# Performance work log

Hardware: AMD Instinct MI355X
Metric: run time of the kernel (lower is better)

The kernel has to match this reference:

```python
import jax, jax.numpy as jnp
import numpy as np


def setup_inputs() -> dict:
    key = jax.random.key(0)
    ks = jax.random.split(key, 5)
    B, S, D = 2, 2048, 1024
    scale = 0.02
    return {
        "x": jax.random.normal(ks[0], (B, S, D), dtype=jnp.float32),
        "q_proj_weight": jax.random.normal(ks[1], (D, D), dtype=jnp.float32) * scale,
        "k_proj_weight": jax.random.normal(ks[2], (D, D), dtype=jnp.float32) * scale,
        "v_proj_weight": jax.random.normal(ks[3], (D, D), dtype=jnp.float32) * scale,
        "o_proj_weight": jax.random.normal(ks[4], (D, D), dtype=jnp.float32) * scale,
    }


def reference(x, q_proj_weight, k_proj_weight, v_proj_weight, o_proj_weight):
    num_heads = 16
    B, S, d_in = x.shape
    d_k = q_proj_weight.shape[0]
    head_size = d_k // num_heads

    def split_heads(t):  # [B,S,d_k] -> [B,H,S,hs]
        return t.reshape(B, S, num_heads, head_size).transpose(0, 2, 1, 3)

    q = split_heads(jnp.einsum('bsd,kd->bsk', x, q_proj_weight))
    k = split_heads(jnp.einsum('bsd,kd->bsk', x, k_proj_weight))
    v = split_heads(jnp.einsum('bsd,kd->bsk', x, v_proj_weight))

    scale = jnp.float32(head_size) ** -0.5
    scores = jnp.einsum('bhtc,bhkc->bhtk', q, k) * scale  # [B,H,S,S]
    causal = jnp.tril(jnp.ones((S, S), dtype=bool))
    scores = jnp.where(causal, scores, -jnp.inf)
    attn = jax.nn.softmax(scores, axis=-1)
    out = jnp.einsum('bhtk,bhkc->bhtc', attn, v)  # [B,H,S,hs]
    out = out.transpose(0, 2, 1, 3).reshape(B, S, d_k)
    return jnp.einsum('bsv,dv->bsd', out, o_proj_weight)
```

## Files before the change

### kernel.cpp

```cpp
#include <hip/hip_runtime.h>
#include <hip/hip_bf16.h>

typedef short bf16x8 __attribute__((ext_vector_type(8)));
typedef float f32x4 __attribute__((ext_vector_type(4)));

__device__ __forceinline__ short f2bf(float f) {
  union { __hip_bfloat16 h; short s; } u;
  u.h = __float2bfloat16(f);
  return u.s;
}

__device__ __forceinline__ void gload_lds16(const short* g, short* lds_base) {
  __builtin_amdgcn_global_load_lds(
      (const __attribute__((address_space(1))) void*)g,
      (__attribute__((address_space(3))) void*)lds_base, 16, 0, 0);
}

__global__ void cast_f32_bf16(const float* __restrict__ in, short* __restrict__ out, int n4) {
  int i = blockIdx.x * blockDim.x + threadIdx.x;
  if (i < n4) {
    float4 v = reinterpret_cast<const float4*>(in)[i];
    short4 o;
    o.x = f2bf(v.x); o.y = f2bf(v.y); o.z = f2bf(v.z); o.w = f2bf(v.w);
    reinterpret_cast<short4*>(out)[i] = o;
  }
}

__global__ void cast_w4(const float* __restrict__ w0, const float* __restrict__ w1,
                        const float* __restrict__ w2, const float* __restrict__ w3,
                        short* __restrict__ dst, int n4each) {
  int i = blockIdx.x * blockDim.x + threadIdx.x;
  if (i >= n4each) return;
  const float* src = (blockIdx.y == 0) ? w0 : (blockIdx.y == 1) ? w1
                   : (blockIdx.y == 2) ? w2 : w3;
  float4 v = reinterpret_cast<const float4*>(src)[i];
  short4 o;
  o.x = f2bf(v.x); o.y = f2bf(v.y); o.z = f2bf(v.z); o.w = f2bf(v.w);
  reinterpret_cast<short4*>(dst + (size_t)blockIdx.y * 1024 * 1024)[i] = o;
}

#define QSCALE 0.18033688f

template<int MODE>
__global__ __launch_bounds__(512, 1)
void gemm8p(const short* __restrict__ A, const short* __restrict__ Bw,
            short* __restrict__ Qo, short* __restrict__ Ko, short* __restrict__ Vo,
            float* __restrict__ Cf, int M, int N, int Kd)
{
  __shared__ short As[2][256 * 64];
  __shared__ short Bs[2][192 * 64];
  const int tid = threadIdx.x;
  const int wid = tid >> 6, lane = tid & 63;
  const int l16 = lane & 15, lq = lane >> 4;
  const int l = blockIdx.y * 16 + blockIdx.x;
  const int lsw = (l & 7) * 32 + (l >> 3);
  const int bm = (lsw & 15) * 256, bn = (lsw >> 4) * 192;
  const int wr = (wid >> 2) * 128;
  const int wc = (wid & 3) * 48;
  const int lrow = lane >> 3;
  const int scol = ((lane & 7) ^ lrow) * 8;

#define ST_A(slot, k0) do { _Pragma("unroll")                                     \
  for (int j = 0; j < 4; ++j) {                                                   \
    int r = j * 64 + wid * 8;                                                     \
    gload_lds16(A + (size_t)(bm + r + lrow) * Kd + (k0) + scol, &As[slot][r * 64]); } } while (0)
#define ST_B(slot, k0) do { _Pragma("unroll")                                     \
  for (int j = 0; j < 3; ++j) {                                                   \
    int r = j * 64 + wid * 8;                                                     \
    gload_lds16(Bw + (size_t)(bn + r + lrow) * Kd + (k0) + scol, &Bs[slot][r * 64]); } } while (0)

  f32x4 acc[8][3];
#pragma unroll
  for (int m = 0; m < 8; ++m)
#pragma unroll
    for (int n = 0; n < 3; ++n) acc[m][n] = (f32x4){0.f, 0.f, 0.f, 0.f};

  const int nt = Kd >> 6;
  ST_A(0, 0);  ST_B(0, 0);
  ST_A(1, 64); ST_B(1, 64);
  asm volatile("s_waitcnt vmcnt(7)" ::: "memory");
  __builtin_amdgcn_s_barrier();
  asm volatile("" ::: "memory");

  bf16x8 af[4][2], bl[2][2], bh1[2];

  for (int t = 0; t < nt; ++t) {
    const int slot = t & 1;
    const int k2 = (t + 2) << 6;
    const bool st = (t + 2) < nt;

#pragma unroll
    for (int ks = 0; ks < 2; ++ks) {
      const int csw = (ks * 32 + lq * 8) ^ ((l16 & 7) << 3);
#pragma unroll
      for (int m = 0; m < 4; ++m)
        af[m][ks] = *(const bf16x8*)&As[slot][(wr + m * 16 + l16) * 64 + csw];
#pragma unroll
      for (int n = 0; n < 2; ++n)
        bl[n][ks] = *(const bf16x8*)&Bs[slot][(wc + n * 16 + l16) * 64 + csw];
    }
    __builtin_amdgcn_s_barrier();
    asm volatile("s_waitcnt lgkmcnt(0)" ::: "memory");
    __builtin_amdgcn_sched_barrier(0);
    __builtin_amdgcn_s_setprio(1);
#pragma unroll
    for (int ks = 0; ks < 2; ++ks)
#pragma unroll
      for (int m = 0; m < 4; ++m)
#pragma unroll
        for (int n = 0; n < 2; ++n)
          acc[m][n] = __builtin_amdgcn_mfma_f32_16x16x32_bf16(af[m][ks], bl[n][ks], acc[m][n], 0, 0, 0);
    __builtin_amdgcn_s_setprio(0);
    asm volatile("" ::: "memory");
    __builtin_amdgcn_s_barrier();
    asm volatile("" ::: "memory");

#pragma unroll
    for (int ks = 0; ks < 2; ++ks) {
      const int csw = (ks * 32 + lq * 8) ^ ((l16 & 7) << 3);
      bh1[ks] = *(const bf16x8*)&Bs[slot][(wc + 32 + l16) * 64 + csw];
    }
    __builtin_amdgcn_s_barrier();
    asm volatile("s_waitcnt lgkmcnt(0)" ::: "memory");
    __builtin_amdgcn_sched_barrier(0);
    __builtin_amdgcn_s_setprio(1);
#pragma unroll
    for (int ks = 0; ks < 2; ++ks)
#pragma unroll
      for (int m = 0; m < 4; ++m)
        acc[m][2] = __builtin_amdgcn_mfma_f32_16x16x32_bf16(af[m][ks], bh1[ks], acc[m][2], 0, 0, 0);
    __builtin_amdgcn_s_setprio(0);
    asm volatile("" ::: "memory");
    __builtin_amdgcn_s_barrier();
    asm volatile("" ::: "memory");

#pragma unroll
    for (int ks = 0; ks < 2; ++ks) {
      const int csw = (ks * 32 + lq * 8) ^ ((l16 & 7) << 3);
#pragma unroll
      for (int m = 0; m < 4; ++m)
        af[m][ks] = *(const bf16x8*)&As[slot][(wr + 64 + m * 16 + l16) * 64 + csw];
    }
    if (st) ST_B(slot, k2);
    __builtin_amdgcn_s_barrier();
    asm volatile("s_waitcnt lgkmcnt(0)" ::: "memory");
    __builtin_amdgcn_sched_barrier(0);
    __builtin_amdgcn_s_setprio(1);
#pragma unroll
    for (int ks = 0; ks < 2; ++ks)
#pragma unroll
      for (int m = 0; m < 4; ++m)
        acc[m + 4][2] = __builtin_amdgcn_mfma_f32_16x16x32_bf16(af[m][ks], bh1[ks], acc[m + 4][2], 0, 0, 0);
    __builtin_amdgcn_s_setprio(0);
    asm volatile("" ::: "memory");
    __builtin_amdgcn_s_barrier();
    asm volatile("" ::: "memory");

    if (st) ST_A(slot, k2);
    __builtin_amdgcn_s_barrier();
    asm volatile("" ::: "memory");
    __builtin_amdgcn_s_setprio(1);
#pragma unroll
    for (int ks = 0; ks < 2; ++ks)
#pragma unroll
      for (int m = 0; m < 4; ++m)
#pragma unroll
        for (int n = 0; n < 2; ++n)
          acc[m + 4][n] = __builtin_amdgcn_mfma_f32_16x16x32_bf16(af[m][ks], bl[n][ks], acc[m + 4][n], 0, 0, 0);
    __builtin_amdgcn_s_setprio(0);
    if (t + 2 < nt)      { asm volatile("s_waitcnt vmcnt(7)" ::: "memory"); }
    else if (t + 1 < nt) { asm volatile("s_waitcnt vmcnt(0)" ::: "memory"); }
    asm volatile("" ::: "memory");
    __builtin_amdgcn_s_barrier();
    asm volatile("" ::: "memory");
  }

#pragma unroll
  for (int m = 0; m < 8; ++m) {
#pragma unroll
    for (int n = 0; n < 3; ++n) {
      int col = bn + wc + n * 16 + l16;
      int rr0 = bm + wr + m * 16 + lq * 4;
      if (MODE == 0) {
        int b = rr0 >> 11;
        int which = col >> 10, cc = col & 1023;
        int h = cc >> 6, d = cc & 63;
        size_t bh2 = (size_t)(b * 16 + h);
        if (which == 2) {
          int s0 = rr0 & 2047;
          short4 pack;
          pack.x = f2bf(acc[m][n][0]); pack.y = f2bf(acc[m][n][1]);
          pack.z = f2bf(acc[m][n][2]); pack.w = f2bf(acc[m][n][3]);
          *reinterpret_cast<short4*>(&Vo[(bh2 * 64 + d) * 2048 + s0]) = pack;
        } else {
#pragma unroll
          for (int i = 0; i < 4; ++i) {
            int s = (rr0 + i) & 2047;
            float v = acc[m][n][i];
            if (which == 0) Qo[(bh2 * 2048 + s) * 64 + d] = f2bf(v * QSCALE);
            else            Ko[(bh2 * 2048 + s) * 64 + d] = f2bf(v);
          }
        }
      } else {
#pragma unroll
        for (int i = 0; i < 4; ++i)
          Cf[(size_t)(rr0 + i) * N + col] = acc[m][n][i];
      }
    }
  }
#undef ST_A
#undef ST_B
}

#define BKT 64

template<int MODE, int TBM, int TBN, int WM, int WN>
__global__ __launch_bounds__(WM * WN * 64, 2)
void gemm_bt(const short* __restrict__ A, const short* __restrict__ Bw,
             float* __restrict__ Cf, int M, int N, int Kd)
{
  constexpr int NWAVE = WM * WN;
  constexpr int MR = TBM / WM / 16;
  constexpr int NR = TBN / WN / 16;
  constexpr int SROWS = TBM / NWAVE;
  constexpr int SITER = SROWS / 8;

  __shared__ short As[2][TBM * BKT];
  __shared__ short Bs[2][TBN * BKT];
  const int tid = threadIdx.x;
  const int wid = tid >> 6, lane = tid & 63;
  const int l16 = lane & 15, lq = lane >> 4;
  const int bm = blockIdx.x * TBM, bn = blockIdx.y * TBN;
  const int wr = (wid / WN) * (TBM / WM);
  const int wc = (wid % WN) * (TBN / WN);

  const int srow = wid * SROWS;
  const int lrow = lane >> 3;
  const int scol = ((lane & 7) ^ lrow) * 8;

#define GSTAGE(buf, k0) do {                                                        \
  _Pragma("unroll")                                                                 \
  for (int j = 0; j < SITER; ++j) {                                                 \
    int r = srow + j * 8;                                                           \
    gload_lds16(A  + (size_t)(bm + r + lrow) * Kd + (k0) + scol, &As[buf][r * BKT]);\
    gload_lds16(Bw + (size_t)(bn + r + lrow) * Kd + (k0) + scol, &Bs[buf][r * BKT]);\
  }                                                                                 \
} while (0)

#define GCOMPUTE(buf) do {                                                          \
  _Pragma("unroll")                                                                 \
  for (int ks = 0; ks < 2; ++ks) {                                                  \
    const int csw = (ks * 32 + lq * 8) ^ ((l16 & 7) << 3);                          \
    bf16x8 af2[MR], bfr[NR];                                                        \
    _Pragma("unroll")                                                               \
    for (int m = 0; m < MR; ++m)                                                    \
      af2[m] = *reinterpret_cast<const bf16x8*>(                                    \
          &As[buf][(wr + m * 16 + l16) * BKT + csw]);                               \
    _Pragma("unroll")                                                               \
    for (int n = 0; n < NR; ++n)                                                    \
      bfr[n] = *reinterpret_cast<const bf16x8*>(                                    \
          &Bs[buf][(wc + n * 16 + l16) * BKT + csw]);                               \
    _Pragma("unroll")                                                               \
    for (int m = 0; m < MR; ++m)                                                    \
      _Pragma("unroll")                                                             \
      for (int n = 0; n < NR; ++n)                                                  \
        acc[m][n] = __builtin_amdgcn_mfma_f32_16x16x32_bf16(af2[m], bfr[n], acc[m][n], 0, 0, 0); \
  }                                                                                 \
} while (0)

  f32x4 acc[MR][NR];
#pragma unroll
  for (int m = 0; m < MR; ++m)
#pragma unroll
    for (int n = 0; n < NR; ++n) acc[m][n] = (f32x4){0.f, 0.f, 0.f, 0.f};

  const int nt = Kd >> 6;
  GSTAGE(0, 0);
  for (int t = 0; t < nt; ++t) {
    const int cur = t & 1;
    if (t + 1 < nt) {
      GSTAGE(cur ^ 1, (t + 1) << 6);
      asm volatile("s_waitcnt vmcnt(%0)" :: "i"(2 * SITER) : "memory");
    } else {
      asm volatile("s_waitcnt vmcnt(0)" ::: "memory");
    }
    __builtin_amdgcn_s_barrier();
    asm volatile("" ::: "memory");
    GCOMPUTE(cur);
    asm volatile("" ::: "memory");
    __builtin_amdgcn_s_barrier();
    asm volatile("" ::: "memory");
  }

#pragma unroll
  for (int m = 0; m < MR; ++m)
#pragma unroll
    for (int n = 0; n < NR; ++n) {
      int col = bn + wc + n * 16 + l16;
      int rr0 = bm + wr + m * 16 + lq * 4;
#pragma unroll
      for (int i = 0; i < 4; ++i)
        Cf[(size_t)(rr0 + i) * N + col] = acc[m][n][i];
    }
#undef GSTAGE
#undef GCOMPUTE
}

__global__ __launch_bounds__(256)
void attn_fwd(const short* __restrict__ Qb, const short* __restrict__ Kb,
              const short* __restrict__ Vb, short* __restrict__ Ob)
{
  constexpr int S = 2048, HS = 64;
  constexpr float SM2 = 17.3123405f;
  __shared__ short Ks[2][64][72];
  __shared__ short Vs[2][64][72];
  __shared__ short Ps[4][16][72];

  const int tid = threadIdx.x;
  const int wid = tid >> 6, lane = tid & 63;
  const int l16 = lane & 15, lq = lane >> 4;
  const int qt = gridDim.y - 1 - blockIdx.y;
  const int bh = blockIdx.x;

  const short* Qp = Qb + ((size_t)bh * S + qt * 64) * HS;
  const short* Kp = Kb + (size_t)bh * S * HS;
  const short* Vp = Vb + (size_t)bh * HS * S;

  bf16x8 qf[2];
#pragma unroll
  for (int ks = 0; ks < 2; ++ks)
    qf[ks] = *reinterpret_cast<const bf16x8*>(Qp + (wid * 16 + l16) * HS + ks * 32 + lq * 8);

  f32x4 oacc[4];
#pragma unroll
  for (int t = 0; t < 4; ++t) oacc[t] = (f32x4){0.f, 0.f, 0.f, 0.f};
  float lrow[4] = {0.f, 0.f, 0.f, 0.f};

  const int qrow_base = qt * 64 + wid * 16 + lq * 4;
  const int sr = tid >> 3;
  const int so = (tid & 7) * 8;

  bf16x8 kreg[2], vreg[2];

#define LOADKV(kt) do {                                                            \
  _Pragma("unroll")                                                                \
  for (int i2 = 0; i2 < 2; ++i2) {                                                 \
    kreg[i2] = *reinterpret_cast<const bf16x8*>(Kp + (size_t)((kt) * 64 + sr + 32 * i2) * HS + so); \
    vreg[i2] = *reinterpret_cast<const bf16x8*>(Vp + (size_t)(sr + 32 * i2) * S + (kt) * 64 + so);  \
  }                                                                                \
} while (0)

#define WRITEKV(buf) do {                                                          \
  _Pragma("unroll")                                                                \
  for (int i2 = 0; i2 < 2; ++i2) {                                                 \
    *reinterpret_cast<bf16x8*>(&Ks[buf][sr + 32 * i2][so]) = kreg[i2];             \
    *reinterpret_cast<bf16x8*>(&Vs[buf][sr + 32 * i2][so]) = vreg[i2];             \
  }                                                                                \
} while (0)

  LOADKV(0);
  WRITEKV(0);
  __syncthreads();

  for (int kt = 0; kt <= qt; ++kt) {
    const int buf = kt & 1;
    if (kt + 1 <= qt) LOADKV(kt + 1);

    f32x4 sacc[4];
#pragma unroll
    for (int n = 0; n < 4; ++n) sacc[n] = (f32x4){0.f, 0.f, 0.f, 0.f};
#pragma unroll
    for (int ks = 0; ks < 2; ++ks) {
#pragma unroll
      for (int n = 0; n < 4; ++n) {
        bf16x8 kf = *reinterpret_cast<const bf16x8*>(&Ks[buf][n * 16 + l16][ks * 32 + lq * 8]);
        sacc[n] = __builtin_amdgcn_mfma_f32_16x16x32_bf16(qf[ks], kf, sacc[n], 0, 0, 0);
      }
    }

    const bool diag = (kt == qt);
#pragma unroll
    for (int i = 0; i < 4; ++i) {
      const int qrow = qrow_base + i;
      float psum = 0.f;
#pragma unroll
      for (int n = 0; n < 4; ++n) {
        float v = sacc[n][i];
        if (diag && (kt * 64 + n * 16 + l16) > qrow) v = -1e30f;
        float e = exp2f(v - SM2);
        psum += e;
        Ps[wid][lq * 4 + i][n * 16 + l16] = f2bf(e);
      }
      lrow[i] += psum;
    }

#pragma unroll
    for (int ks = 0; ks < 2; ++ks) {
      bf16x8 pf = *reinterpret_cast<const bf16x8*>(&Ps[wid][l16][ks * 32 + lq * 8]);
#pragma unroll
      for (int t = 0; t < 4; ++t) {
        bf16x8 vf = *reinterpret_cast<const bf16x8*>(&Vs[buf][t * 16 + l16][ks * 32 + lq * 8]);
        oacc[t] = __builtin_amdgcn_mfma_f32_16x16x32_bf16(pf, vf, oacc[t], 0, 0, 0);
      }
    }

    if (kt + 1 <= qt) WRITEKV(buf ^ 1);
    __syncthreads();
  }

  float linv[4];
#pragma unroll
  for (int i = 0; i < 4; ++i) {
    float l = lrow[i];
#pragma unroll
    for (int d = 1; d < 16; d <<= 1) l += __shfl_xor(l, d);
    linv[i] = 1.0f / l;
  }

  const int b = bh >> 4, h = bh & 15;
#pragma unroll
  for (int t = 0; t < 4; ++t)
#pragma unroll
    for (int i = 0; i < 4; ++i) {
      float v = oacc[t][i] * linv[i];
      int srow2 = qt * 64 + wid * 16 + lq * 4 + i;
      int dcol = h * 64 + t * 16 + l16;
      Ob[((size_t)b * S + srow2) * 1024 + dcol] = f2bf(v);
    }
#undef LOADKV
#undef WRITEKV
}

extern "C" void kernel_launch(void* const* d_in, const int* in_sizes, int n_in,
                              void* d_out, int out_size, void* d_ws, size_t ws_size,
                              hipStream_t stream) {
  const float* x   = (const float*)d_in[0];
  const float* wqf = (const float*)d_in[1];
  const float* wkf = (const float*)d_in[2];
  const float* wvf = (const float*)d_in[3];
  const float* wof = (const float*)d_in[4];
  float* out = (float*)d_out;

  short* xb = (short*)d_ws;
  short* wq = xb + (size_t)4096 * 1024;
  short* wk = wq + (size_t)1024 * 1024;
  short* wv = wk + (size_t)1024 * 1024;
  short* wo = wv + (size_t)1024 * 1024;
  short* Qb = wo + (size_t)1024 * 1024;
  short* Kb = Qb + (size_t)32 * 2048 * 64;
  short* Vb = Kb + (size_t)32 * 2048 * 64;
  short* Ob = Vb + (size_t)32 * 2048 * 64;

  cast_f32_bf16<<<4096, 256, 0, stream>>>(x, xb, 4096 * 1024 / 4);
  cast_w4<<<dim3(1024, 4), 256, 0, stream>>>(wqf, wkf, wvf, wof, wq, 1024 * 1024 / 4);

  gemm8p<0><<<dim3(16, 16), 512, 0, stream>>>(xb, wq, Qb, Kb, Vb, nullptr, 4096, 3072, 1024);

  attn_fwd<<<dim3(32, 32), 256, 0, stream>>>(Qb, Kb, Vb, Ob);

  gemm_bt<2, 128, 128, 2, 2><<<dim3(32, 8), 256, 0, stream>>>(
      Ob, wo, out, 4096, 1024, 1024);
}
```

Baseline: 113.1 us.

## Process two adjacent query tiles per attention block to reuse K/V tiles

Each attention block now handles two adjacent 64-row query tiles (2j+1 and 2j) and shares every K/V tile it loads between them, which halves the grid along the query dimension. This is meant to cut global K/V traffic and LDS staging per unit of work. The cost is more registers for two accumulator sets, fewer blocks in flight (512 instead of 1024), and serialised use of the shared P buffer within each iteration. Because the kernel uses fixed-offset exp without a running max, the softmax maths is unchanged.

```diff
diff --git a/kernel.cpp b/kernel.cpp
--- a/kernel.cpp
+++ b/kernel.cpp
@@ -319,24 +319,34 @@
   const int tid = threadIdx.x;
   const int wid = tid >> 6, lane = tid & 63;
   const int l16 = lane & 15, lq = lane >> 4;
-  const int qt = gridDim.y - 1 - blockIdx.y;
+  const int jp = 15 - blockIdx.y;
+  const int qtA = 2 * jp + 1, qtB = 2 * jp;
   const int bh = blockIdx.x;
 
-  const short* Qp = Qb + ((size_t)bh * S + qt * 64) * HS;
+  const short* Qp = Qb + (size_t)bh * S * HS;
   const short* Kp = Kb + (size_t)bh * S * HS;
   const short* Vp = Vb + (size_t)bh * HS * S;
 
-  bf16x8 qf[2];
-#pragma unroll
-  for (int ks = 0; ks < 2; ++ks)
-    qf[ks] = *reinterpret_cast<const bf16x8*>(Qp + (wid * 16 + l16) * HS + ks * 32 + lq * 8);
-
-  f32x4 oacc[4];
-#pragma unroll
-  for (int t = 0; t < 4; ++t) oacc[t] = (f32x4){0.f, 0.f, 0.f, 0.f};
-  float lrow[4] = {0.f, 0.f, 0.f, 0.f};
-
-  const int qrow_base = qt * 64 + wid * 16 + lq * 4;
+  bf16x8 qfA[2], qfB[2];
+#pragma unroll
+  for (int ks = 0; ks < 2; ++ks) {
+    qfA[ks] = *reinterpret_cast<const bf16x8*>(
+        Qp + (size_t)(qtA * 64 + wid * 16 + l16) * HS + ks * 32 + lq * 8);
+    qfB[ks] = *reinterpret_cast<const bf16x8*>(
+        Qp + (size_t)(qtB * 64 + wid * 16 + l16) * HS + ks * 32 + lq * 8);
+  }
+
+  f32x4 oaccA[4], oaccB[4];
+#pragma unroll
+  for (int t = 0; t < 4; ++t) {
+    oaccA[t] = (f32x4){0.f, 0.f, 0.f, 0.f};
+    oaccB[t] = (f32x4){0.f, 0.f, 0.f, 0.f};
+  }
+  float lrowA[4] = {0.f, 0.f, 0.f, 0.f};
+  float lrowB[4] = {0.f, 0.f, 0.f, 0.f};
+
+  const int qrbA = qtA * 64 + wid * 16 + lq * 4;
+  const int qrbB = qtB * 64 + wid * 16 + lq * 4;
   const int sr = tid >> 3;
   const int so = (tid & 7) * 8;
 
@@ -362,71 +372,132 @@
   WRITEKV(0);
   __syncthreads();
 
-  for (int kt = 0; kt <= qt; ++kt) {
+  for (int kt = 0; kt <= qtA; ++kt) {
     const int buf = kt & 1;
-    if (kt + 1 <= qt) LOADKV(kt + 1);
-
-    f32x4 sacc[4];
-#pragma unroll
-    for (int n = 0; n < 4; ++n) sacc[n] = (f32x4){0.f, 0.f, 0.f, 0.f};
-#pragma unroll
-    for (int ks = 0; ks < 2; ++ks) {
-#pragma unroll
-      for (int n = 0; n < 4; ++n) {
-        bf16x8 kf = *reinterpret_cast<const bf16x8*>(&Ks[buf][n * 16 + l16][ks * 32 + lq * 8]);
-        sacc[n] = __builtin_amdgcn_mfma_f32_16x16x32_bf16(qf[ks], kf, sacc[n], 0, 0, 0);
-      }
-    }
-
-    const bool diag = (kt == qt);
+    if (kt < qtA) LOADKV(kt + 1);
+
+    bf16x8 kf[2][4];
+#pragma unroll
+    for (int ks = 0; ks < 2; ++ks)
+#pragma unroll
+      for (int n = 0; n < 4; ++n)
+        kf[ks][n] = *reinterpret_cast<const bf16x8*>(&Ks[buf][n * 16 + l16][ks * 32 + lq * 8]);
+
+    f32x4 saccA[4], saccB[4];
+#pragma unroll
+    for (int n = 0; n < 4; ++n) {
+      saccA[n] = (f32x4){0.f, 0.f, 0.f, 0.f};
+      saccB[n] = (f32x4){0.f, 0.f, 0.f, 0.f};
+    }
+    const bool act = (kt <= qtB);
+#pragma unroll
+    for (int ks = 0; ks < 2; ++ks)
+#pragma unroll
+      for (int n = 0; n < 4; ++n)
+        saccA[n] = __builtin_amdgcn_mfma_f32_16x16x32_bf16(qfA[ks], kf[ks][n], saccA[n], 0, 0, 0);
+    if (act) {
+#pragma unroll
+      for (int ks = 0; ks < 2; ++ks)
+#pragma unroll
+        for (int n = 0; n < 4; ++n)
+          saccB[n] = __builtin_amdgcn_mfma_f32_16x16x32_bf16(qfB[ks], kf[ks][n], saccB[n], 0, 0, 0);
+    }
+
+    {
+      const bool diag = (kt == qtA);
+#pragma unroll
+      for (int i = 0; i < 4; ++i) {
+        const int qrow = qrbA + i;
+        float psum = 0.f;
+#pragma unroll
+        for (int n = 0; n < 4; ++n) {
+          float v = saccA[n][i];
+          if (diag && (kt * 64 + n * 16 + l16) > qrow) v = -1e30f;
+          float e = exp2f(v - SM2);
+          psum += e;
+          Ps[wid][lq * 4 + i][n * 16 + l16] = f2bf(e);
+        }
+        lrowA[i] += psum;
+      }
+#pragma unroll
+      for (int ks = 0; ks < 2; ++ks) {
+        bf16x8 pf = *reinterpret_cast<const bf16x8*>(&Ps[wid][l16][ks * 32 + lq * 8]);
+#pragma unroll
+        for (int t = 0; t < 4; ++t) {
+          bf16x8 vf = *reinterpret_cast<const bf16x8*>(&Vs[buf][t * 16 + l16][ks * 32 + lq * 8]);
+          oaccA[t] = __builtin_amdgcn_mfma_f32_16x16x32_bf16(pf, vf, oaccA[t], 0, 0, 0);
+        }
+      }
+    }
+
+    if (act) {
+      const bool diag = (kt == qtB);
+#pragma unroll
+      for (int i = 0; i < 4; ++i) {
+        const int qrow = qrbB + i;
+        float psum = 0.f;
+#pragma unroll
+        for (int n = 0; n < 4; ++n) {
+          float v = saccB[n][i];
+          if (diag && (kt * 64 + n * 16 + l16) > qrow) v = -1e30f;
+          float e = exp2f(v - SM2);
+          psum += e;
+          Ps[wid][lq * 4 + i][n * 16 + l16] = f2bf(e);
+        }
+        lrowB[i] += psum;
+      }
+#pragma unroll
+      for (int ks = 0; ks < 2; ++ks) {
+        bf16x8 pf = *reinterpret_cast<const bf16x8*>(&Ps[wid][l16][ks * 32 + lq * 8]);
+#pragma unroll
+        for (int t = 0; t < 4; ++t) {
+          bf16x8 vf = *reinterpret_cast<const bf16x8*>(&Vs[buf][t * 16 + l16][ks * 32 + lq * 8]);
+          oaccB[t] = __builtin_amdgcn_mfma_f32_16x16x32_bf16(pf, vf, oaccB[t], 0, 0, 0);
+        }
+      }
+    }
+
+    if (kt < qtA) WRITEKV(buf ^ 1);
+    __syncthreads();
+  }
+
+  const int b = bh >> 4, h = bh & 15;
+  {
+    float linv[4];
 #pragma unroll
     for (int i = 0; i < 4; ++i) {
-      const int qrow = qrow_base + i;
-      float psum = 0.f;
-#pragma unroll
-      for (int n = 0; n < 4; ++n) {
-        float v = sacc[n][i];
-        if (diag && (kt * 64 + n * 16 + l16) > qrow) v = -1e30f;
-        float e = exp2f(v - SM2);
-        psum += e;
-        Ps[wid][lq * 4 + i][n * 16 + l16] = f2bf(e);
-      }
-      lrow[i] += psum;
-    }
-
-#pragma unroll
-    for (int ks = 0; ks < 2; ++ks) {
-      bf16x8 pf = *reinterpret_cast<const bf16x8*>(&Ps[wid][l16][ks * 32 + lq * 8]);
-#pragma unroll
-      for (int t = 0; t < 4; ++t) {
-        bf16x8 vf = *reinterpret_cast<const bf16x8*>(&Vs[buf][t * 16 + l16][ks * 32 + lq * 8]);
-        oacc[t] = __builtin_amdgcn_mfma_f32_16x16x32_bf16(pf, vf, oacc[t], 0, 0, 0);
-      }
-    }
-
-    if (kt + 1 <= qt) WRITEKV(buf ^ 1);
-    __syncthreads();
-  }
-
-  float linv[4];
-#pragma unroll
-  for (int i = 0; i < 4; ++i) {
-    float l = lrow[i];
-#pragma unroll
-    for (int d = 1; d < 16; d <<= 1) l += __shfl_xor(l, d);
-    linv[i] = 1.0f / l;
-  }
-
-  const int b = bh >> 4, h = bh & 15;
-#pragma unroll
-  for (int t = 0; t < 4; ++t)
+      float l = lrowA[i];
+#pragma unroll
+      for (int d = 1; d < 16; d <<= 1) l += __shfl_xor(l, d);
+      linv[i] = 1.0f / l;
+    }
+#pragma unroll
+    for (int t = 0; t < 4; ++t)
+#pragma unroll
+      for (int i = 0; i < 4; ++i) {
+        int srow2 = qtA * 64 + wid * 16 + lq * 4 + i;
+        int dcol = h * 64 + t * 16 + l16;
+        Ob[((size_t)b * S + srow2) * 1024 + dcol] = f2bf(oaccA[t][i] * linv[i]);
+      }
+  }
+  {
+    float linv[4];
 #pragma unroll
     for (int i = 0; i < 4; ++i) {
-      float v = oacc[t][i] * linv[i];
-      int srow2 = qt * 64 + wid * 16 + lq * 4 + i;
-      int dcol = h * 64 + t * 16 + l16;
-      Ob[((size_t)b * S + srow2) * 1024 + dcol] = f2bf(v);
-    }
+      float l = lrowB[i];
+#pragma unroll
+      for (int d = 1; d < 16; d <<= 1) l += __shfl_xor(l, d);
+      linv[i] = 1.0f / l;
+    }
+#pragma unroll
+    for (int t = 0; t < 4; ++t)
+#pragma unroll
+      for (int i = 0; i < 4; ++i) {
+        int srow2 = qtB * 64 + wid * 16 + lq * 4 + i;
+        int dcol = h * 64 + t * 16 + l16;
+        Ob[((size_t)b * S + srow2) * 1024 + dcol] = f2bf(oaccB[t][i] * linv[i]);
+      }
+  }
 #undef LOADKV
 #undef WRITEKV
 }
@@ -456,7 +527,7 @@
 
   gemm8p<0><<<dim3(16, 16), 512, 0, stream>>>(xb, wq, Qb, Kb, Vb, nullptr, 4096, 3072, 1024);
 
-  attn_fwd<<<dim3(32, 32), 256, 0, stream>>>(Qb, Kb, Vb, Ob);
+  attn_fwd<<<dim3(32, 16), 256, 0, stream>>>(Qb, Kb, Vb, Ob);
 
   gemm_bt<2, 128, 128, 2, 2><<<dim3(32, 8), 256, 0, stream>>>(
       Ob, wo, out, 4096, 1024, 1024);
```

Result: slower. 127.8 us (+13.0%).
